# Kernel optimization log

Measured on AMD Instinct MI355X. Metric: run time of the kernel, lower is better.

## Reference

```python
import jax, jax.numpy as jnp
import numpy as np

TEMPERATURE = 0.5
N, D = 8192, 256
N_CLASSES = 64


def setup_inputs() -> dict:
    key = jax.random.key(0)
    k1, k2 = jax.random.split(key)
    emb = jax.random.normal(k1, (N, D), dtype=jnp.float32)
    # original module expects normalized embeddings
    emb = emb / jnp.linalg.norm(emb, axis=-1, keepdims=True)
    labels = jax.random.randint(k2, (N,), 0, N_CLASSES, dtype=jnp.int64)
    return {"embeddings": emb, "epitope_labels": labels}


def reference(embeddings, epitope_labels):
    n = embeddings.shape[0]
    # [N, N] pairwise similarities
    sim = jnp.matmul(embeddings, embeddings.T) / TEMPERATURE
    eye = jnp.eye(n, dtype=bool)
    labels_eq = epitope_labels[None, :] == epitope_labels[:, None]
    mask_pos = labels_eq & ~eye  # positives exclude self
    # row-max subtraction (detached, matches torch .detach())
    sim_max = jax.lax.stop_gradient(jnp.max(sim, axis=1, keepdims=True))
    shifted = sim - sim_max
    exp_sim = jnp.exp(shifted)
    # denominator excludes the diagonal (self-similarity)
    denom = jnp.sum(jnp.where(eye, 0.0, exp_sim), axis=1)  # [N]
    # per-pair loss: -log(exp_sim_ij / denom_i) = -(shifted_ij - log denom_i)
    per_pair = -(shifted - jnp.log(denom)[:, None])
    # mean over positive pairs (equivalent to masked_select + repeat_interleave + mean)
    n_pos = jnp.sum(mask_pos)
    loss = jnp.sum(jnp.where(mask_pos, per_pair, 0.0)) / n_pos
    return loss
```

## Files before the change

kernel.cpp:

```cpp
#include <hip/hip_runtime.h>
#include <hip/hip_bf16.h>

#define N 8192
#define D 256

typedef __attribute__((ext_vector_type(8))) short bf16x8;
typedef __attribute__((ext_vector_type(4))) float f32x4;

#define BM 128
#define BN 64
#define COLS_PER_BLK 512
#define NT (COLS_PER_BLK / BN)
#define ROWBLKS (N / BM)
#define COLBLKS (N / COLS_PER_BLK)

#define K1 2.8853900817779268f
#define K2 (-2.8853900817779268f)

__device__ inline unsigned short f2bf(float x) {
    __hip_bfloat16 h = __float2bfloat16(x);
    return *reinterpret_cast<unsigned short*>(&h);
}

__device__ inline float fast_exp2(float t) {
#if __has_builtin(__builtin_amdgcn_exp2f)
    return __builtin_amdgcn_exp2f(t);
#else
    return __expf(t * 0.69314718056f);
#endif
}

__global__ void convert_kernel(const float4* __restrict__ E4, ushort4* __restrict__ Ebf4,
                               float* __restrict__ Z, float* __restrict__ P,
                               float* __restrict__ nd) {
    int i = blockIdx.x * blockDim.x + threadIdx.x;
    int n4 = (N * D) / 4;
    if (i < n4) {
        float4 v = E4[i];
        ushort4 o;
        o.x = f2bf(v.x); o.y = f2bf(v.y); o.z = f2bf(v.z); o.w = f2bf(v.w);
        Ebf4[i] = o;
    }
    if (i < N) { Z[i] = 0.0f; P[i] = 0.0f; }
    if (i < 2) nd[i] = 0.0f;
}

__global__ __launch_bounds__(256)
void sim_kernel(const __hip_bfloat16* __restrict__ Ebf,
                const int* __restrict__ labels,
                float* __restrict__ Z, float* __restrict__ P) {
    __shared__ unsigned char Bsh[BN * 512];
    __shared__ int Lcol[COLS_PER_BLK];

    const int tid  = threadIdx.x;
    const int lane = tid & 63;
    const int wid  = tid >> 6;
    const int blk  = blockIdx.x;
    const int r0   = (blk >> 4) * BM;
    const int c0   = (blk & 15) * COLS_PER_BLK;

    for (int t = tid; t < COLS_PER_BLK; t += 256) Lcol[t] = labels[c0 + t];

    const char* ebase = (const char*)Ebf;

    bf16x8 a[2][8];
#pragma unroll
    for (int rg = 0; rg < 2; ++rg) {
        int row = r0 + wid * 32 + rg * 16 + (lane & 15);
        const char* rp = ebase + (size_t)row * (D * 2) + ((lane >> 4) * 16);
#pragma unroll
        for (int kg = 0; kg < 8; ++kg)
            a[rg][kg] = *reinterpret_cast<const bf16x8*>(rp + kg * 64);
    }

    int labi[2][4];
#pragma unroll
    for (int rg = 0; rg < 2; ++rg)
#pragma unroll
        for (int r = 0; r < 4; ++r)
            labi[rg][r] = labels[r0 + wid * 32 + rg * 16 + (lane >> 4) * 4 + r];

    unsigned rbase[4];
#pragma unroll
    for (int cg = 0; cg < 4; ++cg) {
        unsigned col = cg * 16 + (lane & 15);
        unsigned seg = lane >> 4;
        rbase[cg] = (col * 64 + seg * 16) ^ (((col >> 1) & 3) << 4);
    }

    float zacc[2][4] = {{0}}, pacc[2][4] = {{0}};

    for (int ct = 0; ct < NT; ++ct) {
        __syncthreads();
#pragma unroll
        for (int m = 0; m < 8; ++m) {
            int c = wid * 8 + m;
            int kg = c >> 2, colblk = c & 3;
            unsigned dbase = kg * 4096 + colblk * 1024;
            int colLocal = colblk * 16 + (lane >> 2);
            int seg_src  = (lane & 3) ^ ((colLocal >> 1) & 3);
            const char* src = ebase + (size_t)(c0 + ct * 64 + colLocal) * 512
                            + kg * 64 + seg_src * 16;
            __builtin_amdgcn_global_load_lds(
                (const __attribute__((address_space(1))) void*)src,
                (__attribute__((address_space(3))) void*)(Bsh + dbase), 16, 0, 0);
        }
        __syncthreads();

        f32x4 acc[2][4];
#pragma unroll
        for (int rg = 0; rg < 2; ++rg)
#pragma unroll
            for (int cg = 0; cg < 4; ++cg) acc[rg][cg] = (f32x4){0.f, 0.f, 0.f, 0.f};

#pragma unroll
        for (int cg = 0; cg < 4; ++cg) {
#pragma unroll
            for (int kg = 0; kg < 8; ++kg) {
                bf16x8 b = *reinterpret_cast<const bf16x8*>(Bsh + rbase[cg] + kg * 4096);
                acc[0][cg] = __builtin_amdgcn_mfma_f32_16x16x32_bf16(a[0][kg], b, acc[0][cg], 0, 0, 0);
                acc[1][cg] = __builtin_amdgcn_mfma_f32_16x16x32_bf16(a[1][kg], b, acc[1][cg], 0, 0, 0);
            }
        }

#pragma unroll
        for (int cg = 0; cg < 4; ++cg) {
            int labj = Lcol[ct * 64 + cg * 16 + (lane & 15)];
#pragma unroll
            for (int rg = 0; rg < 2; ++rg)
#pragma unroll
                for (int r = 0; r < 4; ++r) {
                    float d = acc[rg][cg][r];
                    zacc[rg][r] += fast_exp2(__builtin_fmaf(d, K1, K2));
                    pacc[rg][r] += (labi[rg][r] == labj) ? d : 0.0f;
                }
        }
    }

#pragma unroll
    for (int rg = 0; rg < 2; ++rg)
#pragma unroll
        for (int r = 0; r < 4; ++r) {
            float z = zacc[rg][r], p = pacc[rg][r];
#pragma unroll
            for (int m = 1; m <= 8; m <<= 1) {
                z += __shfl_xor(z, m, 64);
                p += __shfl_xor(p, m, 64);
            }
            if ((lane & 15) == 0) {
                int i = r0 + wid * 32 + rg * 16 + (lane >> 4) * 4 + r;
                atomicAdd(&Z[i], z);
                atomicAdd(&P[i], p);
            }
        }
}

__global__ void finalize_kernel(const float* __restrict__ Z, const float* __restrict__ P,
                                const int* __restrict__ labels, float* __restrict__ nd) {
    __shared__ int hist[64];
    __shared__ float snum[256], sden[256];
    int t = threadIdx.x;
    if (t < 64) hist[t] = 0;
    __syncthreads();
    for (int i = t; i < N; i += 256) atomicAdd(&hist[labels[i]], 1);
    __syncthreads();

    int i = blockIdx.x * 256 + t;
    float z = Z[i] - 1.0f;
    float p = 2.0f * (P[i] - 1.0f);
    float c = (float)(hist[labels[i]] - 1);
    float num = c * (2.0f + __logf(z)) - p;
    float den = c;

    snum[t] = num; sden[t] = den;
    __syncthreads();
    for (int s = 128; s > 0; s >>= 1) {
        if (t < s) { snum[t] += snum[t + s]; sden[t] += sden[t + s]; }
        __syncthreads();
    }
    if (t == 0) { atomicAdd(&nd[0], snum[0]); atomicAdd(&nd[1], sden[0]); }
}

__global__ void div_kernel(const float* __restrict__ nd, float* __restrict__ out) {
    out[0] = nd[0] / nd[1];
}

extern "C" void kernel_launch(void* const* d_in, const int* in_sizes, int n_in,
                              void* d_out, int out_size, void* d_ws, size_t ws_size,
                              hipStream_t stream) {
    const float* emb  = (const float*)d_in[0];
    const int* labels = (const int*)d_in[1];
    float* out = (float*)d_out;

    char* ws = (char*)d_ws;
    __hip_bfloat16* Ebf = (__hip_bfloat16*)ws;
    float* Z  = (float*)(ws + (size_t)N * D * 2);
    float* P  = Z + N;
    float* nd = P + N;

    convert_kernel<<<(N * D / 4 + 255) / 256, 256, 0, stream>>>(
        (const float4*)emb, (ushort4*)Ebf, Z, P, nd);
    sim_kernel<<<ROWBLKS * COLBLKS, 256, 0, stream>>>(Ebf, labels, Z, P);
    finalize_kernel<<<N / 256, 256, 0, stream>>>(Z, P, labels, nd);
    div_kernel<<<1, 1, 0, stream>>>(nd, out);
}
```

Measured before the change: 113.2 us.

## Exploit similarity symmetry with upper-triangular persistent tiling and double-buffered staging

Computes only the upper-triangular 128x32 tiles of the symmetric similarity matrix. Each off-diagonal tile feeds both row sums and column sums, which roughly halves the MFMA and exp work. Tiles are spread evenly over a fixed grid of 1024 blocks of 128 threads, and each block decodes its tile indices with a closed-form inverse of the cumulative count. B tiles are double-buffered with async LDS loads so the next tile's load overlaps compute. The finalize and divide kernels are merged into one single-block kernel, which removes a launch. The cost is extra column-side atomics, label packing into bytes (valid because there are 64 classes), and more registers for the A fragments.

```diff
diff --git a/kernel.cpp b/kernel.cpp
--- a/kernel.cpp
+++ b/kernel.cpp
@@ -7,12 +7,12 @@
 typedef __attribute__((ext_vector_type(8))) short bf16x8;
 typedef __attribute__((ext_vector_type(4))) float f32x4;
 
-#define BM 128
-#define BN 64
-#define COLS_PER_BLK 512
-#define NT (COLS_PER_BLK / BN)
-#define ROWBLKS (N / BM)
-#define COLBLKS (N / COLS_PER_BLK)
+#define RB 128
+#define CTW 32
+#define NRB (N / RB)
+#define NTILES 8320
+#define GRID 1024
+#define TPB 128
 
 #define K1 2.8853900817779268f
 #define K2 (-2.8853900817779268f)
@@ -30,159 +30,213 @@
 #endif
 }
 
+__device__ inline int cumtiles(int rb) { return 2 * rb * (129 - rb); }
+
+__device__ inline void decode_tile(int k, int& rb, int& ct) {
+    float f = 64.5f - sqrtf(4160.25f - 0.5f * (float)k);
+    rb = (int)f;
+    if (rb < 0) rb = 0;
+    if (rb > 63) rb = 63;
+    while (rb < 63 && cumtiles(rb + 1) <= k) ++rb;
+    while (rb > 0 && cumtiles(rb) > k) --rb;
+    ct = rb * 4 + (k - cumtiles(rb));
+}
+
 __global__ void convert_kernel(const float4* __restrict__ E4, ushort4* __restrict__ Ebf4,
-                               float* __restrict__ Z, float* __restrict__ P,
-                               float* __restrict__ nd) {
+                               float* __restrict__ Z, float* __restrict__ P) {
     int i = blockIdx.x * blockDim.x + threadIdx.x;
-    int n4 = (N * D) / 4;
-    if (i < n4) {
+    if (i < (N * D) / 4) {
         float4 v = E4[i];
         ushort4 o;
         o.x = f2bf(v.x); o.y = f2bf(v.y); o.z = f2bf(v.z); o.w = f2bf(v.w);
         Ebf4[i] = o;
     }
     if (i < N) { Z[i] = 0.0f; P[i] = 0.0f; }
-    if (i < 2) nd[i] = 0.0f;
-}
-
-__global__ __launch_bounds__(256)
+}
+
+__global__ __launch_bounds__(TPB, 2)
 void sim_kernel(const __hip_bfloat16* __restrict__ Ebf,
                 const int* __restrict__ labels,
                 float* __restrict__ Z, float* __restrict__ P) {
-    __shared__ unsigned char Bsh[BN * 512];
-    __shared__ int Lcol[COLS_PER_BLK];
+    __shared__ unsigned char Bsh[2 * 16384];
 
     const int tid  = threadIdx.x;
     const int lane = tid & 63;
-    const int wid  = tid >> 6;
-    const int blk  = blockIdx.x;
-    const int r0   = (blk >> 4) * BM;
-    const int c0   = (blk & 15) * COLS_PER_BLK;
-
-    for (int t = tid; t < COLS_PER_BLK; t += 256) Lcol[t] = labels[c0 + t];
-
-    const char* ebase = (const char*)Ebf;
-
-    bf16x8 a[2][8];
-#pragma unroll
-    for (int rg = 0; rg < 2; ++rg) {
-        int row = r0 + wid * 32 + rg * 16 + (lane & 15);
-        const char* rp = ebase + (size_t)row * (D * 2) + ((lane >> 4) * 16);
-#pragma unroll
-        for (int kg = 0; kg < 8; ++kg)
-            a[rg][kg] = *reinterpret_cast<const bf16x8*>(rp + kg * 64);
-    }
-
-    int labi[2][4];
-#pragma unroll
-    for (int rg = 0; rg < 2; ++rg)
-#pragma unroll
-        for (int r = 0; r < 4; ++r)
-            labi[rg][r] = labels[r0 + wid * 32 + rg * 16 + (lane >> 4) * 4 + r];
-
-    unsigned rbase[4];
-#pragma unroll
-    for (int cg = 0; cg < 4; ++cg) {
-        unsigned col = cg * 16 + (lane & 15);
-        unsigned seg = lane >> 4;
-        rbase[cg] = (col * 64 + seg * 16) ^ (((col >> 1) & 3) << 4);
-    }
-
-    float zacc[2][4] = {{0}}, pacc[2][4] = {{0}};
-
-    for (int ct = 0; ct < NT; ++ct) {
-        __syncthreads();
+    const int w    = tid >> 6;
+    const int bid  = blockIdx.x;
+
+    const int k0 = (int)(((long long)bid * NTILES) / GRID);
+    const int k1 = (int)(((long long)(bid + 1) * NTILES) / GRID);
+
+    const char* eb = (const char*)Ebf;
+
+    bf16x8 a[4][8];
+    int labP[4];
+    float zacc[4][4], pacc[4][4];
+    int prev_rb = -1;
+    int cur = 0;
+
+    auto stage = [&](int buf, int ct) {
 #pragma unroll
         for (int m = 0; m < 8; ++m) {
-            int c = wid * 8 + m;
-            int kg = c >> 2, colblk = c & 3;
-            unsigned dbase = kg * 4096 + colblk * 1024;
+            int c = w * 8 + m;
+            int kg = c >> 1, colblk = c & 1;
+            unsigned dbase = (unsigned)buf * 16384u + kg * 2048u + colblk * 1024u;
             int colLocal = colblk * 16 + (lane >> 2);
-            int seg_src  = (lane & 3) ^ ((colLocal >> 1) & 3);
-            const char* src = ebase + (size_t)(c0 + ct * 64 + colLocal) * 512
-                            + kg * 64 + seg_src * 16;
+            int seg = (lane & 3) ^ ((colLocal >> 1) & 3);
+            const char* src = eb + (size_t)(ct * CTW + colLocal) * 512 + kg * 64 + seg * 16;
             __builtin_amdgcn_global_load_lds(
                 (const __attribute__((address_space(1))) void*)src,
                 (__attribute__((address_space(3))) void*)(Bsh + dbase), 16, 0, 0);
         }
-        __syncthreads();
-
-        f32x4 acc[2][4];
-#pragma unroll
-        for (int rg = 0; rg < 2; ++rg)
-#pragma unroll
-            for (int cg = 0; cg < 4; ++cg) acc[rg][cg] = (f32x4){0.f, 0.f, 0.f, 0.f};
-
-#pragma unroll
-        for (int cg = 0; cg < 4; ++cg) {
-#pragma unroll
-            for (int kg = 0; kg < 8; ++kg) {
-                bf16x8 b = *reinterpret_cast<const bf16x8*>(Bsh + rbase[cg] + kg * 4096);
-                acc[0][cg] = __builtin_amdgcn_mfma_f32_16x16x32_bf16(a[0][kg], b, acc[0][cg], 0, 0, 0);
-                acc[1][cg] = __builtin_amdgcn_mfma_f32_16x16x32_bf16(a[1][kg], b, acc[1][cg], 0, 0, 0);
-            }
-        }
-
-#pragma unroll
-        for (int cg = 0; cg < 4; ++cg) {
-            int labj = Lcol[ct * 64 + cg * 16 + (lane & 15)];
-#pragma unroll
-            for (int rg = 0; rg < 2; ++rg)
+    };
+
+    auto flush_rows = [&](int rb) {
+#pragma unroll
+        for (int rg = 0; rg < 4; ++rg)
+#pragma unroll
+            for (int r = 0; r < 4; ++r) {
+                float z = zacc[rg][r], p = pacc[rg][r];
+#pragma unroll
+                for (int m = 1; m <= 8; m <<= 1) {
+                    z += __shfl_xor(z, m, 64);
+                    p += __shfl_xor(p, m, 64);
+                }
+                if ((lane & 15) == 0) {
+                    int row = rb * RB + w * 64 + rg * 16 + (lane >> 4) * 4 + r;
+                    atomicAdd(&Z[row], z);
+                    atomicAdd(&P[row], p);
+                }
+            }
+    };
+
+    {
+        int rb0, ct0;
+        decode_tile(k0, rb0, ct0);
+        stage(0, ct0);
+    }
+    __syncthreads();
+
+    for (int k = k0; k < k1; ++k) {
+        int rb, ct;
+        decode_tile(k, rb, ct);
+
+        if (rb != prev_rb) {
+            if (prev_rb >= 0) flush_rows(prev_rb);
+#pragma unroll
+            for (int rg = 0; rg < 4; ++rg) {
+                int arow = rb * RB + w * 64 + rg * 16 + (lane & 15);
+                const char* rp = eb + (size_t)arow * 512 + ((lane >> 4) * 16);
+#pragma unroll
+                for (int kg = 0; kg < 8; ++kg)
+                    a[rg][kg] = *reinterpret_cast<const bf16x8*>(rp + kg * 64);
+                int rr = rb * RB + w * 64 + rg * 16 + (lane >> 4) * 4;
+                labP[rg] = labels[rr] | (labels[rr + 1] << 8) |
+                           (labels[rr + 2] << 16) | (labels[rr + 3] << 24);
+                for (int r = 0; r < 4; ++r) { zacc[rg][r] = 0.0f; pacc[rg][r] = 0.0f; }
+            }
+            prev_rb = rb;
+        }
+
+        if (k + 1 < k1) {
+            int rbn, ctn;
+            decode_tile(k + 1, rbn, ctn);
+            stage(cur ^ 1, ctn);
+        }
+
+        int labj[2];
+#pragma unroll
+        for (int cg = 0; cg < 2; ++cg)
+            labj[cg] = labels[ct * CTW + cg * 16 + (lane & 15)];
+
+        unsigned rbase[2];
+#pragma unroll
+        for (int cg = 0; cg < 2; ++cg) {
+            unsigned col = cg * 16 + (lane & 15);
+            rbase[cg] = (unsigned)cur * 16384u + col * 64u
+                      + ((((unsigned)(lane >> 4)) ^ ((col >> 1) & 3u)) << 4);
+        }
+
+        f32x4 acc[4][2];
+#pragma unroll
+        for (int rg = 0; rg < 4; ++rg)
+#pragma unroll
+            for (int cg = 0; cg < 2; ++cg) acc[rg][cg] = (f32x4){0.f, 0.f, 0.f, 0.f};
+
+#pragma unroll
+        for (int kg = 0; kg < 8; ++kg) {
+            bf16x8 b0 = *reinterpret_cast<const bf16x8*>(Bsh + rbase[0] + kg * 2048);
+            bf16x8 b1 = *reinterpret_cast<const bf16x8*>(Bsh + rbase[1] + kg * 2048);
+#pragma unroll
+            for (int rg = 0; rg < 4; ++rg) {
+                acc[rg][0] = __builtin_amdgcn_mfma_f32_16x16x32_bf16(a[rg][kg], b0, acc[rg][0], 0, 0, 0);
+                acc[rg][1] = __builtin_amdgcn_mfma_f32_16x16x32_bf16(a[rg][kg], b1, acc[rg][1], 0, 0, 0);
+            }
+        }
+
+        const bool colpath = (ct >= rb * 4 + 4);
+        float zc[2] = {0.f, 0.f}, pc[2] = {0.f, 0.f};
+#pragma unroll
+        for (int cg = 0; cg < 2; ++cg)
+#pragma unroll
+            for (int rg = 0; rg < 4; ++rg)
 #pragma unroll
                 for (int r = 0; r < 4; ++r) {
                     float d = acc[rg][cg][r];
-                    zacc[rg][r] += fast_exp2(__builtin_fmaf(d, K1, K2));
-                    pacc[rg][r] += (labi[rg][r] == labj) ? d : 0.0f;
-                }
-        }
-    }
-
-#pragma unroll
-    for (int rg = 0; rg < 2; ++rg)
-#pragma unroll
-        for (int r = 0; r < 4; ++r) {
-            float z = zacc[rg][r], p = pacc[rg][r];
-#pragma unroll
-            for (int m = 1; m <= 8; m <<= 1) {
-                z += __shfl_xor(z, m, 64);
-                p += __shfl_xor(p, m, 64);
-            }
-            if ((lane & 15) == 0) {
-                int i = r0 + wid * 32 + rg * 16 + (lane >> 4) * 4 + r;
-                atomicAdd(&Z[i], z);
-                atomicAdd(&P[i], p);
-            }
-        }
-}
-
-__global__ void finalize_kernel(const float* __restrict__ Z, const float* __restrict__ P,
-                                const int* __restrict__ labels, float* __restrict__ nd) {
+                    float e = fast_exp2(__builtin_fmaf(d, K1, K2));
+                    zacc[rg][r] += e;
+                    int lr = (labP[rg] >> (r * 8)) & 255;
+                    float t = (lr == labj[cg]) ? d : 0.0f;
+                    pacc[rg][r] += t;
+                    zc[cg] += e;
+                    pc[cg] += t;
+                }
+
+        if (colpath) {
+#pragma unroll
+            for (int cg = 0; cg < 2; ++cg) {
+                float z = zc[cg], p = pc[cg];
+                z += __shfl_xor(z, 16, 64); z += __shfl_xor(z, 32, 64);
+                p += __shfl_xor(p, 16, 64); p += __shfl_xor(p, 32, 64);
+                if (lane < 16) {
+                    int col = ct * CTW + cg * 16 + lane;
+                    atomicAdd(&Z[col], z);
+                    atomicAdd(&P[col], p);
+                }
+            }
+        }
+
+        __syncthreads();
+        cur ^= 1;
+    }
+    if (prev_rb >= 0) flush_rows(prev_rb);
+}
+
+__global__ __launch_bounds__(1024)
+void finalize_kernel(const float* __restrict__ Z, const float* __restrict__ P,
+                     const int* __restrict__ labels, float* __restrict__ out) {
     __shared__ int hist[64];
-    __shared__ float snum[256], sden[256];
+    __shared__ float s0[1024], s1[1024];
     int t = threadIdx.x;
     if (t < 64) hist[t] = 0;
     __syncthreads();
-    for (int i = t; i < N; i += 256) atomicAdd(&hist[labels[i]], 1);
-    __syncthreads();
-
-    int i = blockIdx.x * 256 + t;
-    float z = Z[i] - 1.0f;
-    float p = 2.0f * (P[i] - 1.0f);
-    float c = (float)(hist[labels[i]] - 1);
-    float num = c * (2.0f + __logf(z)) - p;
-    float den = c;
-
-    snum[t] = num; sden[t] = den;
-    __syncthreads();
-    for (int s = 128; s > 0; s >>= 1) {
-        if (t < s) { snum[t] += snum[t + s]; sden[t] += sden[t + s]; }
+    for (int i = t; i < N; i += 1024) atomicAdd(&hist[labels[i]], 1);
+    __syncthreads();
+    float num = 0.0f, den = 0.0f;
+    for (int i = t; i < N; i += 1024) {
+        float z = Z[i] - 1.0f;
+        float p = 2.0f * (P[i] - 1.0f);
+        float c = (float)(hist[labels[i]] - 1);
+        num += c * (2.0f + __logf(z)) - p;
+        den += c;
+    }
+    s0[t] = num; s1[t] = den;
+    __syncthreads();
+    for (int s = 512; s > 0; s >>= 1) {
+        if (t < s) { s0[t] += s0[t + s]; s1[t] += s1[t + s]; }
         __syncthreads();
     }
-    if (t == 0) { atomicAdd(&nd[0], snum[0]); atomicAdd(&nd[1], sden[0]); }
-}
-
-__global__ void div_kernel(const float* __restrict__ nd, float* __restrict__ out) {
-    out[0] = nd[0] / nd[1];
+    if (t == 0) out[0] = s0[0] / s1[0];
 }
 
 extern "C" void kernel_launch(void* const* d_in, const int* in_sizes, int n_in,
@@ -194,13 +248,11 @@
 
     char* ws = (char*)d_ws;
     __hip_bfloat16* Ebf = (__hip_bfloat16*)ws;
-    float* Z  = (float*)(ws + (size_t)N * D * 2);
-    float* P  = Z + N;
-    float* nd = P + N;
+    float* Z = (float*)(ws + (size_t)N * D * 2);
+    float* P = Z + N;
 
     convert_kernel<<<(N * D / 4 + 255) / 256, 256, 0, stream>>>(
-        (const float4*)emb, (ushort4*)Ebf, Z, P, nd);
-    sim_kernel<<<ROWBLKS * COLBLKS, 256, 0, stream>>>(Ebf, labels, Z, P);
-    finalize_kernel<<<N / 256, 256, 0, stream>>>(Z, P, labels, nd);
-    div_kernel<<<1, 1, 0, stream>>>(nd, out);
-}
+        (const float4*)emb, (ushort4*)Ebf, Z, P);
+    sim_kernel<<<GRID, TPB, 0, stream>>>(Ebf, labels, Z, P);
+    finalize_kernel<<<1, 1024, 0, stream>>>(Z, P, labels, out);
+}
```

After: 117.2 us. +3.5%, slower.

## Compute positive-pair sum via class-sum norms; double-buffer and enlarge sim tiles

Applied to the files above, without the earlier changes.

The positive-pair similarity sum is replaced by an algebraic identity: the sum of squared norms of per-class embedding sums, computed by a new class-sum kernel. This drops the label comparisons from the GEMM epilogue. The sim kernel now uses 256-row blocks with a double-buffered LDS pipeline that prefetches the next column tile during compute, and the finalize and div kernels are merged into one single-block kernel. In exchange it adds an extra kernel pass over the fp32 embeddings plus atomics into a 64x256 buffer. The positive sum is now taken from fp32 class sums rather than the bf16 GEMM, so its rounding differs from before.

```diff
diff --git a/kernel.cpp b/kernel.cpp
--- a/kernel.cpp
+++ b/kernel.cpp
@@ -3,16 +3,15 @@
 
 #define N 8192
 #define D 256
+#define NC 64
 
 typedef __attribute__((ext_vector_type(8))) short bf16x8;
 typedef __attribute__((ext_vector_type(4))) float f32x4;
 
-#define BM 128
-#define BN 64
-#define COLS_PER_BLK 512
-#define NT (COLS_PER_BLK / BN)
-#define ROWBLKS (N / BM)
-#define COLBLKS (N / COLS_PER_BLK)
+#define BM 256
+#define CT 64
+#define NTILE 8
+#define GRID 512
 
 #define K1 2.8853900817779268f
 #define K2 (-2.8853900817779268f)
@@ -31,158 +30,171 @@
 }
 
 __global__ void convert_kernel(const float4* __restrict__ E4, ushort4* __restrict__ Ebf4,
-                               float* __restrict__ Z, float* __restrict__ P,
-                               float* __restrict__ nd) {
+                               float* __restrict__ Z, float* __restrict__ S) {
     int i = blockIdx.x * blockDim.x + threadIdx.x;
-    int n4 = (N * D) / 4;
-    if (i < n4) {
+    if (i < (N * D) / 4) {
         float4 v = E4[i];
         ushort4 o;
         o.x = f2bf(v.x); o.y = f2bf(v.y); o.z = f2bf(v.z); o.w = f2bf(v.w);
         Ebf4[i] = o;
     }
-    if (i < N) { Z[i] = 0.0f; P[i] = 0.0f; }
-    if (i < 2) nd[i] = 0.0f;
+    if (i < N) Z[i] = 0.0f;
+    if (i < NC * D) S[i] = 0.0f;
 }
 
 __global__ __launch_bounds__(256)
-void sim_kernel(const __hip_bfloat16* __restrict__ Ebf,
-                const int* __restrict__ labels,
-                float* __restrict__ Z, float* __restrict__ P) {
-    __shared__ unsigned char Bsh[BN * 512];
-    __shared__ int Lcol[COLS_PER_BLK];
+void classsum_kernel(const float* __restrict__ emb, const int* __restrict__ labels,
+                     float* __restrict__ S) {
+    __shared__ float Sl[NC * D];
+    int t = threadIdx.x;
+    for (int i = t; i < NC * D; i += 256) Sl[i] = 0.0f;
+    __syncthreads();
+    int rbase = blockIdx.x * 64;
+    for (int r = 0; r < 64; ++r) {
+        int i = rbase + r;
+        int lab = labels[i];
+        Sl[lab * D + t] += emb[(size_t)i * D + t];
+    }
+    __syncthreads();
+    for (int i = t; i < NC * D; i += 256) atomicAdd(&S[i], Sl[i]);
+}
+
+__global__ __launch_bounds__(256, 2)
+void sim_kernel(const __hip_bfloat16* __restrict__ Ebf, float* __restrict__ Z) {
+    __shared__ unsigned char Bsh[2 * 32768];
 
     const int tid  = threadIdx.x;
     const int lane = tid & 63;
-    const int wid  = tid >> 6;
-    const int blk  = blockIdx.x;
-    const int r0   = (blk >> 4) * BM;
-    const int c0   = (blk & 15) * COLS_PER_BLK;
-
-    for (int t = tid; t < COLS_PER_BLK; t += 256) Lcol[t] = labels[c0 + t];
-
-    const char* ebase = (const char*)Ebf;
-
-    bf16x8 a[2][8];
-#pragma unroll
-    for (int rg = 0; rg < 2; ++rg) {
-        int row = r0 + wid * 32 + rg * 16 + (lane & 15);
-        const char* rp = ebase + (size_t)row * (D * 2) + ((lane >> 4) * 16);
+    const int w    = tid >> 6;
+    const int r0   = (blockIdx.x >> 4) * BM;
+    const int c0   = (blockIdx.x & 15) * (CT * NTILE);
+    const char* eb = (const char*)Ebf;
+
+    bf16x8 a[4][8];
+#pragma unroll
+    for (int rg = 0; rg < 4; ++rg) {
+        int row = r0 + w * 64 + rg * 16 + (lane & 15);
+        const char* rp = eb + (size_t)row * 512 + ((lane >> 4) * 16);
 #pragma unroll
         for (int kg = 0; kg < 8; ++kg)
             a[rg][kg] = *reinterpret_cast<const bf16x8*>(rp + kg * 64);
     }
 
-    int labi[2][4];
-#pragma unroll
-    for (int rg = 0; rg < 2; ++rg)
-#pragma unroll
-        for (int r = 0; r < 4; ++r)
-            labi[rg][r] = labels[r0 + wid * 32 + rg * 16 + (lane >> 4) * 4 + r];
-
-    unsigned rbase[4];
-#pragma unroll
-    for (int cg = 0; cg < 4; ++cg) {
-        unsigned col = cg * 16 + (lane & 15);
-        unsigned seg = lane >> 4;
-        rbase[cg] = (col * 64 + seg * 16) ^ (((col >> 1) & 3) << 4);
-    }
-
-    float zacc[2][4] = {{0}}, pacc[2][4] = {{0}};
-
-    for (int ct = 0; ct < NT; ++ct) {
+    float zacc[4][4];
+#pragma unroll
+    for (int rg = 0; rg < 4; ++rg)
+#pragma unroll
+        for (int r = 0; r < 4; ++r) zacc[rg][r] = 0.0f;
+
+    const int seg = (lane & 3) ^ ((lane >> 3) & 3);
+    const char* sbase = eb + (size_t)(c0 + (lane >> 2)) * 512 + seg * 16;
+
+    const unsigned rb0 =
+        (unsigned)((lane & 15) * 64 +
+                   (((lane >> 4) ^ (((lane & 15) >> 1) & 3)) << 4));
+
+    auto stage = [&](int buf, int t) {
+#pragma unroll
+        for (int m = 0; m < 8; ++m) {
+            int c = w * 8 + m;
+            int kg = c >> 2, colblk = c & 3;
+            __builtin_amdgcn_global_load_lds(
+                (const __attribute__((address_space(1))) void*)
+                    (sbase + (size_t)t * (CT * 512) + colblk * 8192 + kg * 64),
+                (__attribute__((address_space(3))) void*)
+                    (Bsh + buf * 32768 + kg * 4096 + colblk * 1024),
+                16, 0, 0);
+        }
+    };
+
+    auto do_tile = [&](int t, int buf) {
+        if (t + 1 < NTILE) stage(buf ^ 1, t + 1);
+
+        f32x4 acc[4][4];
+#pragma unroll
+        for (int rg = 0; rg < 4; ++rg)
+#pragma unroll
+            for (int cg = 0; cg < 4; ++cg) acc[rg][cg] = (f32x4){0.f, 0.f, 0.f, 0.f};
+
+#pragma unroll
+        for (int kg = 0; kg < 8; ++kg) {
+            bf16x8 b[4];
+#pragma unroll
+            for (int cg = 0; cg < 4; ++cg)
+                b[cg] = *reinterpret_cast<const bf16x8*>(
+                    Bsh + buf * 32768 + kg * 4096 + cg * 1024 + rb0);
+#pragma unroll
+            for (int rg = 0; rg < 4; ++rg)
+#pragma unroll
+                for (int cg = 0; cg < 4; ++cg)
+                    acc[rg][cg] = __builtin_amdgcn_mfma_f32_16x16x32_bf16(
+                        a[rg][kg], b[cg], acc[rg][cg], 0, 0, 0);
+        }
+
+#pragma unroll
+        for (int rg = 0; rg < 4; ++rg)
+#pragma unroll
+            for (int r = 0; r < 4; ++r) {
+                float s = zacc[rg][r];
+#pragma unroll
+                for (int cg = 0; cg < 4; ++cg)
+                    s += fast_exp2(__builtin_fmaf(acc[rg][cg][r], K1, K2));
+                zacc[rg][r] = s;
+            }
+
         __syncthreads();
-#pragma unroll
-        for (int m = 0; m < 8; ++m) {
-            int c = wid * 8 + m;
-            int kg = c >> 2, colblk = c & 3;
-            unsigned dbase = kg * 4096 + colblk * 1024;
-            int colLocal = colblk * 16 + (lane >> 2);
-            int seg_src  = (lane & 3) ^ ((colLocal >> 1) & 3);
-            const char* src = ebase + (size_t)(c0 + ct * 64 + colLocal) * 512
-                            + kg * 64 + seg_src * 16;
-            __builtin_amdgcn_global_load_lds(
-                (const __attribute__((address_space(1))) void*)src,
-                (__attribute__((address_space(3))) void*)(Bsh + dbase), 16, 0, 0);
-        }
-        __syncthreads();
-
-        f32x4 acc[2][4];
-#pragma unroll
-        for (int rg = 0; rg < 2; ++rg)
-#pragma unroll
-            for (int cg = 0; cg < 4; ++cg) acc[rg][cg] = (f32x4){0.f, 0.f, 0.f, 0.f};
-
-#pragma unroll
-        for (int cg = 0; cg < 4; ++cg) {
-#pragma unroll
-            for (int kg = 0; kg < 8; ++kg) {
-                bf16x8 b = *reinterpret_cast<const bf16x8*>(Bsh + rbase[cg] + kg * 4096);
-                acc[0][cg] = __builtin_amdgcn_mfma_f32_16x16x32_bf16(a[0][kg], b, acc[0][cg], 0, 0, 0);
-                acc[1][cg] = __builtin_amdgcn_mfma_f32_16x16x32_bf16(a[1][kg], b, acc[1][cg], 0, 0, 0);
+    };
+
+    stage(0, 0);
+    __syncthreads();
+    for (int t = 0; t < NTILE; t += 2) {
+        do_tile(t, 0);
+        do_tile(t + 1, 1);
+    }
+
+#pragma unroll
+    for (int rg = 0; rg < 4; ++rg)
+#pragma unroll
+        for (int r = 0; r < 4; ++r) {
+            float z = zacc[rg][r];
+#pragma unroll
+            for (int m = 1; m <= 8; m <<= 1) z += __shfl_xor(z, m, 64);
+            if ((lane & 15) == 0) {
+                int row = r0 + w * 64 + rg * 16 + (lane >> 4) * 4 + r;
+                atomicAdd(&Z[row], z);
             }
         }
-
-#pragma unroll
-        for (int cg = 0; cg < 4; ++cg) {
-            int labj = Lcol[ct * 64 + cg * 16 + (lane & 15)];
-#pragma unroll
-            for (int rg = 0; rg < 2; ++rg)
-#pragma unroll
-                for (int r = 0; r < 4; ++r) {
-                    float d = acc[rg][cg][r];
-                    zacc[rg][r] += fast_exp2(__builtin_fmaf(d, K1, K2));
-                    pacc[rg][r] += (labi[rg][r] == labj) ? d : 0.0f;
-                }
-        }
-    }
-
-#pragma unroll
-    for (int rg = 0; rg < 2; ++rg)
-#pragma unroll
-        for (int r = 0; r < 4; ++r) {
-            float z = zacc[rg][r], p = pacc[rg][r];
-#pragma unroll
-            for (int m = 1; m <= 8; m <<= 1) {
-                z += __shfl_xor(z, m, 64);
-                p += __shfl_xor(p, m, 64);
-            }
-            if ((lane & 15) == 0) {
-                int i = r0 + wid * 32 + rg * 16 + (lane >> 4) * 4 + r;
-                atomicAdd(&Z[i], z);
-                atomicAdd(&P[i], p);
-            }
-        }
-}
-
-__global__ void finalize_kernel(const float* __restrict__ Z, const float* __restrict__ P,
-                                const int* __restrict__ labels, float* __restrict__ nd) {
-    __shared__ int hist[64];
-    __shared__ float snum[256], sden[256];
+}
+
+__global__ __launch_bounds__(1024)
+void finalize_kernel(const float* __restrict__ Z, const float* __restrict__ S,
+                     const int* __restrict__ labels, float* __restrict__ out) {
+    __shared__ int hist[NC];
+    __shared__ float s0[1024], s1[1024];
     int t = threadIdx.x;
-    if (t < 64) hist[t] = 0;
-    __syncthreads();
-    for (int i = t; i < N; i += 256) atomicAdd(&hist[labels[i]], 1);
-    __syncthreads();
-
-    int i = blockIdx.x * 256 + t;
-    float z = Z[i] - 1.0f;
-    float p = 2.0f * (P[i] - 1.0f);
-    float c = (float)(hist[labels[i]] - 1);
-    float num = c * (2.0f + __logf(z)) - p;
-    float den = c;
-
-    snum[t] = num; sden[t] = den;
-    __syncthreads();
-    for (int s = 128; s > 0; s >>= 1) {
-        if (t < s) { snum[t] += snum[t + s]; sden[t] += sden[t + s]; }
+    if (t < NC) hist[t] = 0;
+    __syncthreads();
+    for (int i = t; i < N; i += 1024) atomicAdd(&hist[labels[i]], 1);
+    __syncthreads();
+
+    float num = 0.0f, den = 0.0f;
+    for (int i = t; i < N; i += 1024) {
+        float z = Z[i] - 1.0f;
+        float c = (float)(hist[labels[i]] - 1);
+        num += c * (2.0f + __logf(z));
+        den += c;
+    }
+    float ss = 0.0f;
+    for (int i = t; i < NC * D; i += 1024) { float v = S[i]; ss += v * v; }
+    num -= 2.0f * ss / 1.0f;
+
+    s0[t] = num; s1[t] = den;
+    __syncthreads();
+    for (int s = 512; s > 0; s >>= 1) {
+        if (t < s) { s0[t] += s0[t + s]; s1[t] += s1[t + s]; }
         __syncthreads();
     }
-    if (t == 0) { atomicAdd(&nd[0], snum[0]); atomicAdd(&nd[1], sden[0]); }
-}
-
-__global__ void div_kernel(const float* __restrict__ nd, float* __restrict__ out) {
-    out[0] = nd[0] / nd[1];
+    if (t == 0) out[0] = (s0[0] + 2.0f * (float)N) / s1[0];
 }
 
 extern "C" void kernel_launch(void* const* d_in, const int* in_sizes, int n_in,
@@ -194,13 +206,12 @@
 
     char* ws = (char*)d_ws;
     __hip_bfloat16* Ebf = (__hip_bfloat16*)ws;
-    float* Z  = (float*)(ws + (size_t)N * D * 2);
-    float* P  = Z + N;
-    float* nd = P + N;
+    float* Z = (float*)(ws + (size_t)N * D * 2);
+    float* S = Z + N;
 
     convert_kernel<<<(N * D / 4 + 255) / 256, 256, 0, stream>>>(
-        (const float4*)emb, (ushort4*)Ebf, Z, P, nd);
-    sim_kernel<<<ROWBLKS * COLBLKS, 256, 0, stream>>>(Ebf, labels, Z, P);
-    finalize_kernel<<<N / 256, 256, 0, stream>>>(Z, P, labels, nd);
-    div_kernel<<<1, 1, 0, stream>>>(nd, out);
-}
+        (const float4*)emb, (ushort4*)Ebf, Z, S);
+    classsum_kernel<<<N / 64, 256, 0, stream>>>(emb, labels, S);
+    sim_kernel<<<GRID, 256, 0, stream>>>(Ebf, Z);
+    finalize_kernel<<<1, 1024, 0, stream>>>(Z, S, labels, out);
+}
```

New measurement: 123.6 us. 9.2% more time.
